# Kernel tuning notes

Hardware: AMD Instinct MI355X
Metric: run time of the kernel (lower is better)

## Reference

```python
import jax, jax.numpy as jnp
import numpy as np

B, L, K = 4, 2048, 30
NS, NV = 1024, 256   # node hidden (scalar, vector)
ES, EV = 32, 1       # edge hidden (scalar, vector)
CLAMP = 32           # clamp_rel_pos
PE = 16              # num positional embeddings

def _nan_to_num(t):
    return jnp.where(jnp.isfinite(t), t, jnp.zeros((), t.dtype))

def _norm(t, axis=-1, keepdims=False, eps=1e-8):
    return jnp.sqrt(jnp.sum(t * t, axis=axis, keepdims=keepdims) + eps)

def _normalize(t, axis=-1):
    return _nan_to_num(t / _norm(t, axis=axis, keepdims=True))

def _norm_no_nan(t, axis=-1, keepdims=False, eps=1e-8, sqrt=True):
    out = jnp.maximum(jnp.sum(t * t, axis=axis, keepdims=keepdims), eps)
    return jnp.sqrt(out) if sqrt else out

def _rbf(values, v_min, v_max, n_bins=16):
    centers = jnp.linspace(v_min, v_max, n_bins)
    std = (v_max - v_min) / n_bins
    z = (values[..., None] - centers) / std
    return jnp.exp(-z * z)

def _dihedrals(X, eps=1e-7):
    b = X.shape[0]
    Xf = X[:, :, :3].reshape(b, -1, 3)           # [B, 3L, 3]
    U = _normalize(Xf[:, 1:] - Xf[:, :-1])
    u2, u1, u0 = U[:, :-2], U[:, 1:-1], U[:, 2:]
    n2 = _normalize(jnp.cross(u2, u1))
    n1 = _normalize(jnp.cross(u1, u0))
    cosD = jnp.clip(jnp.sum(n2 * n1, -1), -1 + eps, 1 - eps)
    D = jnp.sign(jnp.sum(u2 * n1, -1)) * jnp.arccos(cosD)
    D = jnp.pad(D, ((0, 0), (1, 2))).reshape(b, -1, 3)
    return jnp.concatenate([jnp.cos(D), jnp.sin(D)], -1)   # [B,L,6]

def _orientations(Xca):
    f = jnp.pad(_normalize(Xca[:, 1:] - Xca[:, :-1]), ((0, 0), (0, 1), (0, 0)))
    bk = jnp.pad(_normalize(Xca[:, :-1] - Xca[:, 1:]), ((0, 0), (1, 0), (0, 0)))
    return jnp.concatenate([f[:, :, None], bk[:, :, None]], -2)  # [B,L,2,3]

def _sidechains(X):
    n, origin, c = X[:, :, 0], X[:, :, 1], X[:, :, 2]
    c, n = _normalize(c - origin), _normalize(n - origin)
    bisector = _normalize(c + n)
    perp = _normalize(jnp.cross(c, n))
    return -bisector * float(np.sqrt(1.0 / 3.0)) - perp * float(np.sqrt(2.0 / 3.0))

def _dist(Xca, coord_mask, res_idx, padding_mask, k, order=3):
    n = Xca.shape[1]
    cmf = coord_mask.astype(jnp.float32)
    cm2 = cmf[:, None, :] * cmf[:, :, None]
    rmf = (~padding_mask).astype(jnp.float32)
    rm2 = rmf[:, None, :] * rmf[:, :, None]
    dX = Xca[:, None, :, :] - Xca[:, :, None, :]
    D = cm2 * _norm(dX, axis=-1)
    cov = (jnp.abs(res_idx[:, :, None] - res_idx[:, None, :]) <= order).astype(jnp.float32)
    D_cov = D * (1.0 - cov)
    seqpos = jnp.arange(n)
    Dseq = jnp.abs(seqpos[:, None] - seqpos[None, :]).astype(jnp.float32)
    D_adjust = _nan_to_num(D_cov) + (1.0 - cm2) * (1e8 + Dseq * 1e6) + (1.0 - rm2) * 1e10
    _, E_idx = jax.lax.top_k(-D_adjust, k)                # k smallest
    D_neighbors = jnp.take_along_axis(D, E_idx, axis=-1)  # regather raw D (as in source)
    return D_neighbors, E_idx, D_neighbors < 5e7, D_neighbors < 5e9

def _edge_features(coords, coord_mask, res_idx, padding_mask):
    Xca = coords[:, :, 1]
    E_dist, E_idx, E_cm, E_rm = _dist(Xca, coord_mask, res_idx, padding_mask, K)
    b, n, k = E_idx.shape
    src = jnp.broadcast_to(jnp.arange(n, dtype=E_idx.dtype)[None, :, None], (b, n, k))
    edge_index = jnp.stack([src, E_idx], 0).reshape(2, b, n * k)
    E_dist = E_dist.reshape(b, n * k)
    E_cm = E_cm.reshape(b, n * k)
    E_rm = E_rm.reshape(b, n * k)
    E_cmf = E_cm[..., None].astype(jnp.float32)
    edge_start = jnp.take_along_axis(res_idx, edge_index[0], axis=-1)
    edge_end = jnp.take_along_axis(res_idx, edge_index[1], axis=-1)
    d = jnp.clip(edge_start - edge_end, -CLAMP, CLAMP).astype(jnp.float32)
    freq = jnp.exp(jnp.arange(0, PE, 2, dtype=jnp.float32) * (-np.log(10000.0) / PE))
    ang = d[..., None] * freq
    pos = jnp.concatenate([jnp.cos(ang), jnp.sin(ang)], -1)
    D_rbf = _rbf(E_dist, 0.0, 20.0)
    X_src = jnp.broadcast_to(Xca[:, :, None, :], (b, n, k, 3)).reshape(b, n * k, 3)
    X_dest = jnp.take_along_axis(Xca, edge_index[1][..., None], axis=1)
    cm_src = jnp.broadcast_to(coord_mask[:, :, None], (b, n, k)).reshape(b, n * k)
    cm_dest = jnp.take_along_axis(coord_mask, edge_index[1], axis=1)
    E_vec = X_src - X_dest
    E_mean = jnp.sum(E_vec * E_cmf, 1, keepdims=True) / jnp.sum(E_cmf, 1, keepdims=True)
    E_vec = E_vec * E_cmf + E_mean * (1.0 - E_cmf)
    edge_s = _nan_to_num(jnp.concatenate([D_rbf, pos], -1))
    edge_v = _nan_to_num(_normalize(E_vec)[:, :, None, :])
    edge_s = jnp.concatenate([edge_s,
                              (~cm_src).astype(jnp.float32)[..., None],
                              (~cm_dest).astype(jnp.float32)[..., None]], -1)  # [B,Lk,34]
    invalid = (~E_rm) | (~E_cm)   # remove_edges_without_coords=True
    edge_index = jnp.where(invalid[None], -1, edge_index)
    return edge_s, edge_v, jnp.transpose(edge_index, (1, 0, 2)), invalid

def _gvp(s, v, wh, ws_w, ws_b, wv):
    # v: [..., vi, 3]; activations=(None, None), vector_gate=False
    vh = jnp.einsum('...id,ih->...hd', v, wh)       # [..., h, 3]
    vn = _norm_no_nan(vh, axis=-1)                  # [..., h]
    s_out = jnp.concatenate([s, vn], -1) @ ws_w + ws_b
    v_out = jnp.einsum('...hd,hv->...vd', vh, wv)
    return s_out, v_out

def _gvp_layernorm(s, v, gamma, beta, eps=1e-4):
    mu = jnp.mean(s, -1, keepdims=True)
    var = jnp.mean((s - mu) ** 2, -1, keepdims=True)
    s_out = (s - mu) / jnp.sqrt(var + eps) * gamma + beta
    vn2 = _norm_no_nan(v, axis=-1, keepdims=True, sqrt=False)
    v_out = v / jnp.sqrt(jnp.mean(vn2, axis=-2, keepdims=True))
    return s_out, v_out

def _forward(coords, coord_mask, res_idx, padding_mask, confidence,
             node_wh, node_ws_w, node_ws_b, node_wv, node_ln_g, node_ln_b,
             edge_wh, edge_ws_w, edge_ws_b, edge_wv, edge_ln_g, edge_ln_b,
             conf_w, conf_b):
    node_s = jnp.concatenate([_dihedrals(coords),
                              coord_mask.astype(jnp.float32)[..., None]], -1)  # [B,L,7]
    node_v = jnp.concatenate([_orientations(coords[:, :, 1]),
                              _sidechains(coords)[:, :, None]], -2)            # [B,L,3,3]
    edge_s, edge_v, edge_index, invalid = _edge_features(coords, coord_mask, res_idx, padding_mask)
    # torch.no_grad() over featurization
    node_s, node_v, edge_s, edge_v = map(jax.lax.stop_gradient,
                                         (node_s, node_v, edge_s, edge_v))
    ns, nv = _gvp_layernorm(*_gvp(node_s, node_v, node_wh, node_ws_w, node_ws_b, node_wv),
                            node_ln_g, node_ln_b)
    es, ev = _gvp_layernorm(*_gvp(edge_s, edge_v, edge_wh, edge_ws_w, edge_ws_b, edge_wv),
                            edge_ln_g, edge_ln_b)
    ns = ns + _rbf(confidence, 0.0, 1.0) @ conf_w + conf_b
    b = ns.shape[0]
    ns = ns.reshape(b * L, NS)
    nv = nv.reshape(b * L, NV, 3)
    es = es.reshape(b * L * K, ES)
    ev = ev.reshape(b * L * K, EV, 3)
    # flatten_graph (padded: invalid edges kept with index -1, embeddings zeroed)
    valid = (~invalid).reshape(-1)
    ei = edge_index + (jnp.arange(b, dtype=edge_index.dtype) * L)[:, None, None]
    ei = jnp.transpose(ei, (1, 0, 2)).reshape(2, -1)
    ei = jnp.where(valid[None, :], ei, -1)
    es = jnp.where(valid[:, None], es, 0.0)
    ev = jnp.where(valid[:, None, None], ev, 0.0)
    return ns, nv, es, ev, ei

def setup_inputs():
    key = jax.random.key(0)
    ks = jax.random.split(key, 12)
    def lin(k, fan_in, shape):
        return jax.random.normal(k, shape, jnp.float32) / np.sqrt(fan_in)
    return {
        'coords': jax.random.normal(ks[0], (B, L, 3, 3), jnp.float32),
        'coord_mask': jax.random.randint(ks[1], (B, L), 0, 2) > 0,
        'res_idx': jnp.arange(B * L, dtype=jnp.int32).reshape(B, L),
        'padding_mask': jnp.zeros((B, L), dtype=bool),
        'confidence': jax.random.uniform(ks[2], (B, L), jnp.float32),
        'node_wh': lin(ks[3], 3, (3, NV)),
        'node_ws_w': lin(ks[4], NV + 7, (NV + 7, NS)),
        'node_ws_b': jnp.zeros((NS,), jnp.float32),
        'node_wv': lin(ks[5], NV, (NV, NV)),
        'node_ln_g': jnp.ones((NS,), jnp.float32),
        'node_ln_b': jnp.zeros((NS,), jnp.float32),
        'edge_wh': lin(ks[6], 1, (1, 1)),
        'edge_ws_w': lin(ks[7], 35, (35, ES)),
        'edge_ws_b': jnp.zeros((ES,), jnp.float32),
        'edge_wv': lin(ks[8], 1, (1, 1)),
        'edge_ln_g': jnp.ones((ES,), jnp.float32),
        'edge_ln_b': jnp.zeros((ES,), jnp.float32),
        'conf_w': lin(ks[9], 16, (16, NS)),
        'conf_b': jnp.zeros((NS,), jnp.float32),
    }

def reference(coords, coord_mask, res_idx, padding_mask, confidence,
              node_wh, node_ws_w, node_ws_b, node_wv, node_ln_g, node_ln_b,
              edge_wh, edge_ws_w, edge_ws_b, edge_wv, edge_ln_g, edge_ln_b,
              conf_w, conf_b):
    return _forward(coords, coord_mask, res_idx, padding_mask, confidence,
                    node_wh, node_ws_w, node_ws_b, node_wv, node_ln_g, node_ln_b,
                    edge_wh, edge_ws_w, edge_ws_b, edge_wv, edge_ln_g, edge_ln_b,
                    conf_w, conf_b)
```

## Files before the change

kernel.cpp:

```cpp
#include <hip/hip_runtime.h>
#include <math.h>

constexpr int Bc = 4, Lc = 2048, Kc = 30;
constexpr int Nn = Bc * Lc;
constexpr int NSc = 1024, NVc = 256;
constexpr int NEc = Nn * Kc;
constexpr int SK = 263;

constexpr size_t OUT_NS = 0;
constexpr size_t OUT_NV = (size_t)Nn * NSc;
constexpr size_t OUT_ES = OUT_NV + (size_t)Nn * NVc * 3;
constexpr size_t OUT_EV = OUT_ES + (size_t)NEc * 32;
constexpr size_t OUT_EI = OUT_EV + (size_t)NEc * 3;

constexpr size_t WS_SIN = 0;
constexpr size_t WS_NDV = WS_SIN + (size_t)Nn * SK;
constexpr size_t WS_EIX = WS_NDV + (size_t)Nn * 9;
constexpr size_t WS_EDS = WS_EIX + (size_t)NEc;
constexpr size_t WS_CMF = WS_EDS + (size_t)NEc;

__device__ __forceinline__ void norml3(float& x, float& y, float& z) {
  float ss = x*x + y*y + z*z;
  float inv = 1.0f / sqrtf(ss + 1e-8f);
  x *= inv; y *= inv; z *= inv;
}

__global__ __launch_bounds__(256) void kinit(const unsigned char* __restrict__ cm,
                                             const float* __restrict__ coords,
                                             const int* __restrict__ resid,
                                             const unsigned char* __restrict__ pmask,
                                             const float* __restrict__ wh,
                                             const float* __restrict__ wv,
                                             float* __restrict__ ws,
                                             float4* __restrict__ pack,
                                             float4* __restrict__ whwv4,
                                             float4* __restrict__ wht4) {
  __shared__ float r0[256], r1[256], r2[256];
  __shared__ int flag;
  int tid = threadIdx.x;
  if (blockIdx.x < 32) {
    if (tid == 0) flag = 0;
    __syncthreads();
    int any = 0;
    for (int p = tid; p < 1024; p += 256)
      if (p & 3) any |= cm[p];
    if (any) atomicOr(&flag, 1);
    __syncthreads();
    bool bytefmt = (flag != 0);
    int n = blockIdx.x * 256 + tid;
    unsigned char v = bytefmt ? cm[n] : cm[4*n];
    ws[WS_CMF + n] = v ? 1.f : 0.f;
    int rm = (pmask[n] == 0) ? 1 : 0;
    int w = (resid[n] << 2) | ((v ? 1 : 0) << 1) | rm;
    float4 p;
    p.x = coords[(size_t)n*9 + 3];
    p.y = coords[(size_t)n*9 + 4];
    p.z = coords[(size_t)n*9 + 5];
    p.w = __int_as_float(w);
    pack[n] = p;
  } else {
    int lane = tid & 63, wid = tid >> 6;
    int vcol = (int)(blockIdx.x - 32) * 64 + lane;
    float a0 = 0.f, a1 = 0.f, a2 = 0.f;
    #pragma unroll 4
    for (int hh = 0; hh < 64; ++hh) {
      int h = wid * 64 + hh;
      float wvv = wv[(size_t)h * 256 + vcol];
      a0 = fmaf(wh[h],       wvv, a0);
      a1 = fmaf(wh[256 + h], wvv, a1);
      a2 = fmaf(wh[512 + h], wvv, a2);
    }
    r0[tid] = a0; r1[tid] = a1; r2[tid] = a2;
    __syncthreads();
    if (wid == 0) {
      a0 = r0[lane] + r0[lane+64] + r0[lane+128] + r0[lane+192];
      a1 = r1[lane] + r1[lane+64] + r1[lane+128] + r1[lane+192];
      a2 = r2[lane] + r2[lane+64] + r2[lane+128] + r2[lane+192];
      whwv4[vcol] = float4{a0, a1, a2, 0.f};
    } else if (wid == 1) {
      wht4[vcol] = float4{wh[vcol], wh[256 + vcol], wh[512 + vcol], 0.f};
    }
  }
}

__global__ __launch_bounds__(64) void knode_geom(const float* __restrict__ coords,
                                                 float* __restrict__ ws) {
  int n = blockIdx.x * 64 + threadIdx.x;
  if (n >= Nn) return;
  int b = n / Lc, l = n % Lc;
  const float* Xb = coords + (size_t)b * Lc * 9;
  float ax[7][3];
  #pragma unroll
  for (int m = 0; m < 7; ++m) {
    int t = 3*l + m - 2;
    if (t >= 0 && t < 3*Lc) { ax[m][0]=Xb[t*3+0]; ax[m][1]=Xb[t*3+1]; ax[m][2]=Xb[t*3+2]; }
    else { ax[m][0]=0.f; ax[m][1]=0.f; ax[m][2]=0.f; }
  }
  float U[5][3];
  #pragma unroll
  for (int mi = 0; mi < 5; ++mi) {
    int t = 3*l - 1 + mi;
    if (t >= 0 && t <= 3*Lc - 2) {
      float x = ax[mi+2][0]-ax[mi+1][0], y = ax[mi+2][1]-ax[mi+1][1], z = ax[mi+2][2]-ax[mi+1][2];
      norml3(x,y,z);
      U[mi][0]=x; U[mi][1]=y; U[mi][2]=z;
    } else { U[mi][0]=0.f; U[mi][1]=0.f; U[mi][2]=0.f; }
  }
  float cph[3], sph[3];
  #pragma unroll
  for (int a = 0; a < 3; ++a) {
    int t = 3*l + a - 1;
    if (t < 0 || t > 3*Lc - 4) { cph[a] = 1.f; sph[a] = 0.f; continue; }
    const float *u2 = U[a], *u1 = U[a+1], *u0 = U[a+2];
    float n2x = u2[1]*u1[2]-u2[2]*u1[1], n2y = u2[2]*u1[0]-u2[0]*u1[2], n2z = u2[0]*u1[1]-u2[1]*u1[0];
    norml3(n2x,n2y,n2z);
    float n1x = u1[1]*u0[2]-u1[2]*u0[1], n1y = u1[2]*u0[0]-u1[0]*u0[2], n1z = u1[0]*u0[1]-u1[1]*u0[0];
    norml3(n1x,n1y,n1z);
    float cd = n2x*n1x + n2y*n1y + n2z*n1z;
    cd = fminf(fmaxf(cd, -1.f + 1e-7f), 1.f - 1e-7f);
    float dt = u2[0]*n1x + u2[1]*n1y + u2[2]*n1z;
    float sg = (dt > 0.f) ? 1.f : ((dt < 0.f) ? -1.f : 0.f);
    float D = sg * acosf(cd);
    cph[a] = cosf(D); sph[a] = sinf(D);
  }
  float fx=0.f,fy=0.f,fz=0.f, kx=0.f,ky=0.f,kz=0.f;
  if (l < Lc-1) { fx=ax[6][0]-ax[3][0]; fy=ax[6][1]-ax[3][1]; fz=ax[6][2]-ax[3][2]; norml3(fx,fy,fz); }
  if (l > 0)    { kx=ax[0][0]-ax[3][0]; ky=ax[0][1]-ax[3][1]; kz=ax[0][2]-ax[3][2]; norml3(kx,ky,kz); }
  float cx=ax[4][0]-ax[3][0], cy=ax[4][1]-ax[3][1], cz=ax[4][2]-ax[3][2]; norml3(cx,cy,cz);
  float nx=ax[2][0]-ax[3][0], ny=ax[2][1]-ax[3][1], nz=ax[2][2]-ax[3][2]; norml3(nx,ny,nz);
  float bix=cx+nx, biy=cy+ny, biz=cz+nz; norml3(bix,biy,biz);
  float px=cy*nz-cz*ny, py=cz*nx-cx*nz, pz=cx*ny-cy*nx; norml3(px,py,pz);
  const float c1 = 0.57735026f, c2 = 0.81649658f;
  float sx = -bix*c1 - px*c2, sy = -biy*c1 - py*c2, sz = -biz*c1 - pz*c2;

  float cmf = ws[WS_CMF + n];
  float* sr = ws + WS_SIN + (size_t)n * SK;
  sr[0]=cph[0]; sr[1]=cph[1]; sr[2]=cph[2]; sr[3]=sph[0]; sr[4]=sph[1]; sr[5]=sph[2]; sr[6]=cmf;
  float* vr = ws + WS_NDV + (size_t)n * 9;
  vr[0]=fx; vr[1]=fy; vr[2]=fz; vr[3]=kx; vr[4]=ky; vr[5]=kz; vr[6]=sx; vr[7]=sy; vr[8]=sz;
}

__global__ __launch_bounds__(256) void kvnode(const float4* __restrict__ wht4,
                                              const float4* __restrict__ whwv4,
                                              float* __restrict__ ws,
                                              float* __restrict__ out) {
  int tid = threadIdx.x, lane = tid & 63, wid = tid >> 6;
  int n = blockIdx.x * 4 + wid;
  const float* v = ws + WS_NDV + (size_t)n * 9;
  float v00=v[0],v01=v[1],v02=v[2];
  float v10=v[3],v11=v[4],v12=v[5];
  float v20=v[6],v21=v[7],v22=v[8];
  float p = 0.f;
  float vo[4][3];
  #pragma unroll
  for (int m = 0; m < 4; ++m) {
    int hv = lane + 64*m;
    float4 wt = wht4[hv];
    float vh0 = v00*wt.x + v10*wt.y + v20*wt.z;
    float vh1 = v01*wt.x + v11*wt.y + v21*wt.z;
    float vh2 = v02*wt.x + v12*wt.y + v22*wt.z;
    ws[WS_SIN + (size_t)n*SK + 7 + hv] = sqrtf(fmaxf(vh0*vh0 + vh1*vh1 + vh2*vh2, 1e-8f));
    int ho = lane*4 + m;
    float4 wc = whwv4[ho];
    float o0 = v00*wc.x + v10*wc.y + v20*wc.z;
    float o1 = v01*wc.x + v11*wc.y + v21*wc.z;
    float o2 = v02*wc.x + v12*wc.y + v22*wc.z;
    vo[m][0]=o0; vo[m][1]=o1; vo[m][2]=o2;
    p += fmaxf(o0*o0 + o1*o1 + o2*o2, 1e-8f);
  }
  #pragma unroll
  for (int off = 1; off < 64; off <<= 1) p += __shfl_xor(p, off);
  float isd = 1.f / sqrtf(p * (1.f/256.f));
  size_t o = OUT_NV + (size_t)n*768 + (size_t)lane*12;
  float4 f0 = {vo[0][0]*isd, vo[0][1]*isd, vo[0][2]*isd, vo[1][0]*isd};
  float4 f1 = {vo[1][1]*isd, vo[1][2]*isd, vo[2][0]*isd, vo[2][1]*isd};
  float4 f2 = {vo[2][2]*isd, vo[3][0]*isd, vo[3][1]*isd, vo[3][2]*isd};
  *(float4*)&out[o+0] = f0;
  *(float4*)&out[o+4] = f1;
  *(float4*)&out[o+8] = f2;
}

__global__ __launch_bounds__(256) void ktopk(const float4* __restrict__ pack,
                                             float* __restrict__ ws) {
  __shared__ unsigned long long cbuf[4][256];
  int tid = threadIdx.x, lane = tid & 63, wid = tid >> 6;
  int row = blockIdx.x * 4 + wid;
  int b = row >> 11;
  int i = row & (Lc - 1);
  const float4* P = pack + (size_t)b * Lc;
  int* eix = (int*)(ws + WS_EIX);
  unsigned long long lmask_lt = (1ULL << lane) - 1ULL;

  float4 pi = P[i];
  int wi = __float_as_int(pi.w);
  float cmi = ((wi >> 1) & 1) ? 1.f : 0.f;
  float rmi = (wi & 1) ? 1.f : 0.f;
  int ri = wi >> 2;

  unsigned a[32];
  unsigned lmin = 0xFFFFFFFFu;
  #pragma unroll
  for (int half = 0; half < 2; ++half) {
    float4 pjs[16];
    #pragma unroll
    for (int q = 0; q < 16; ++q)
      pjs[q] = P[lane + 64*(half*16 + q)];
    #pragma unroll
    for (int q = 0; q < 16; ++q) {
      int m = half*16 + q;
      int j = lane + 64*m;
      float4 pj = pjs[q];
      int wj = __float_as_int(pj.w);
      float cmj = ((wj >> 1) & 1) ? 1.f : 0.f;
      float rmj = (wj & 1) ? 1.f : 0.f;
      float dx = __fsub_rn(pi.x, pj.x);
      float dy = __fsub_rn(pi.y, pj.y);
      float dz = __fsub_rn(pi.z, pj.z);
      float ss = __fadd_rn(__fadd_rn(__fmul_rn(dx,dx), __fmul_rn(dy,dy)), __fmul_rn(dz,dz));
      float dist = __fsqrt_rn(__fadd_rn(ss, 1e-8f));
      float cm2 = __fmul_rn(cmi, cmj);
      float D = __fmul_rn(cm2, dist);
      int ad = ri - (wj >> 2); ad = ad < 0 ? -ad : ad;
      float covm = (ad <= 3) ? 0.f : 1.f;
      float dseq = (float)(i >= j ? i - j : j - i);
      float t1 = __fmul_rn(__fsub_rn(1.f, cm2), __fadd_rn(1e8f, __fmul_rn(dseq, 1e6f)));
      float rm2 = __fmul_rn(rmi, rmj);
      float t2 = __fmul_rn(__fsub_rn(1.f, rm2), 1e10f);
      float adj = __fadd_rn(__fadd_rn(__fmul_rn(D, covm), t1), t2);
      unsigned u = __float_as_uint(adj);
      a[m] = u;
      lmin = u < lmin ? u : lmin;
    }
  }

  unsigned lo = 0u, hi = 0x51000000u;
  while (lo < hi) {
    unsigned mid = lo + ((hi - lo) >> 1);
    unsigned long long bal = __ballot(lmin <= mid);
    if (__popcll(bal) >= Kc) hi = mid; else lo = mid + 1u;
  }
  unsigned Tv = lo;

  unsigned base = 0;
  #pragma unroll
  for (int m = 0; m < 32; ++m) {
    bool pred = (a[m] <= Tv);
    unsigned long long bal = __ballot(pred);
    if (pred) {
      unsigned pos = base + (unsigned)__popcll(bal & lmask_lt);
      if (pos < 256u)
        cbuf[wid][pos] = ((unsigned long long)a[m] << 32) | (unsigned)(lane + 64*m);
    }
    base += (unsigned)__popcll(bal);
  }
  unsigned M = base < 256u ? base : 256u;
  __builtin_amdgcn_wave_barrier();

  for (unsigned idx = (unsigned)lane; idx < M; idx += 64u) {
    unsigned long long k0 = cbuf[wid][idx];
    int rank = 0;
    for (unsigned t = 0; t < M; ++t) rank += (cbuf[wid][t] < k0) ? 1 : 0;
    if (rank < Kc) {
      int j = (int)(k0 & 2047ULL);
      float4 pj = P[j];
      int wj = __float_as_int(pj.w);
      float cmj = ((wj >> 1) & 1) ? 1.f : 0.f;
      float dx = __fsub_rn(pi.x, pj.x);
      float dy = __fsub_rn(pi.y, pj.y);
      float dz = __fsub_rn(pi.z, pj.z);
      float ss2 = __fadd_rn(__fadd_rn(__fmul_rn(dx,dx), __fmul_rn(dy,dy)), __fmul_rn(dz,dz));
      float dist = __fsqrt_rn(__fadd_rn(ss2, 1e-8f));
      float D = __fmul_rn(__fmul_rn(cmi, cmj), dist);
      eix[(size_t)row*Kc + rank] = j;
      ws[WS_EDS + (size_t)row*Kc + rank] = D;
    }
  }
}

__global__ __launch_bounds__(256) void kgemm_s(const float* __restrict__ ws,
                                               const float* __restrict__ wsw,
                                               const float* __restrict__ wsb,
                                               float* __restrict__ out) {
  __shared__ __align__(16) float As[32][132];
  __shared__ __align__(16) float Bs[32][64];
  int tid = threadIdx.x;
  int lb = (int)(blockIdx.x & 7) * 128 + (int)(blockIdx.x >> 3);
  int by = lb >> 4, bx = lb & 15;
  int row0 = by * 128, cn0 = bx * 64;
  int tx = tid & 15, ty = tid >> 4;
  int aka = tid & 15, arw = tid >> 4;
  int bkk = tid >> 4, bc4 = tid & 15;
  const float* Abase = ws + WS_SIN;

  float ar[16];
  float4 br[2];
  #pragma unroll
  for (int h = 0; h < 2; ++h) {
    int ka = h*16 + aka;
    #pragma unroll
    for (int i = 0; i < 8; ++i)
      ar[h*8+i] = Abase[(size_t)(row0 + arw + 16*i)*SK + ka];
    br[h] = *(const float4*)&wsw[(size_t)(h*16 + bkk)*NSc + cn0 + bc4*4];
  }
  float acc[8][4] = {};
  for (int k0 = 0; k0 < SK; k0 += 32) {
    #pragma unroll
    for (int h = 0; h < 2; ++h) {
      #pragma unroll
      for (int i = 0; i < 8; ++i)
        As[h*16 + aka][arw + 16*i] = ar[h*8+i];
      *(float4*)&Bs[h*16 + bkk][bc4*4] = br[h];
    }
    __syncthreads();
    int kn = k0 + 32;
    if (kn < SK) {
      #pragma unroll
      for (int h = 0; h < 2; ++h) {
        int ka = kn + h*16 + aka;
        bool ok = (ka < SK);
        #pragma unroll
        for (int i = 0; i < 8; ++i)
          ar[h*8+i] = ok ? Abase[(size_t)(row0 + arw + 16*i)*SK + ka] : 0.f;
        int kb = kn + h*16 + bkk;
        br[h] = (kb < SK) ? *(const float4*)&wsw[(size_t)kb*NSc + cn0 + bc4*4]
                          : float4{0.f,0.f,0.f,0.f};
      }
    }
    #pragma unroll 4
    for (int kk = 0; kk < 32; ++kk) {
      float4 a0 = *(const float4*)&As[kk][ty*8 + 0];
      float4 a1 = *(const float4*)&As[kk][ty*8 + 4];
      float4 b4 = *(const float4*)&Bs[kk][tx*4];
      float av[8] = {a0.x,a0.y,a0.z,a0.w, a1.x,a1.y,a1.z,a1.w};
      float bv[4] = {b4.x,b4.y,b4.z,b4.w};
      #pragma unroll
      for (int r = 0; r < 8; ++r)
        #pragma unroll
        for (int c = 0; c < 4; ++c)
          acc[r][c] = fmaf(av[r], bv[c], acc[r][c]);
    }
    __syncthreads();
  }
  float4 bb = *(const float4*)&wsb[cn0 + tx*4];
  #pragma unroll
  for (int r = 0; r < 8; ++r) {
    size_t o = OUT_NS + (size_t)(row0 + ty*8 + r)*NSc + cn0 + tx*4;
    float4 ov = {acc[r][0]+bb.x, acc[r][1]+bb.y, acc[r][2]+bb.z, acc[r][3]+bb.w};
    *(float4*)&out[o] = ov;
  }
}

__global__ __launch_bounds__(256) void kedge(const float* __restrict__ coords,
    const int* __restrict__ resid,
    const float* __restrict__ ewh, const float* __restrict__ eww,
    const float* __restrict__ ewb, const float* __restrict__ ewv,
    const float* __restrict__ elg, const float* __restrict__ elb,
    const float* __restrict__ ws, float* __restrict__ out) {
  __shared__ float w[35*32];
  __shared__ float wb[32], g[32], bb[32];
  __shared__ float es[256*33];
  int tid = threadIdx.x;
  for (int t = tid; t < 35*32; t += 256) w[t] = eww[t];
  if (tid < 32) { wb[tid] = ewb[tid]; g[tid] = elg[tid]; bb[tid] = elb[tid]; }
  __syncthreads();
  int e = blockIdx.x * 256 + tid;
  int b = e / (Lc*Kc);
  int rem = e - b*(Lc*Kc);
  int i = rem / Kc;
  int row = b*Lc + i;
  const int* eix = (const int*)(ws + WS_EIX);
  int j = eix[e];
  float Dn = ws[WS_EDS + e];
  bool jok = ((unsigned)j < (unsigned)Lc);
  bool valid = jok && (Dn < 5e7f) && (Dn < 5e9f);
  int sj = jok ? j : 0;

  int dcl = resid[row] - resid[b*Lc + sj];
  dcl = dcl < -32 ? -32 : (dcl > 32 ? 32 : dcl);
  float dpos = (float)dcl;
  float s[35];
  #pragma unroll
  for (int m = 0; m < 16; ++m) {
    float c = (20.f/15.f) * (float)m;
    float z = (Dn - c) * 0.8f;
    s[m] = expf(-z*z);
  }
  #pragma unroll
  for (int m = 0; m < 8; ++m) {
    float fr = expf((float)(2*m) * (-0.57564627324851148f));
    float ang = dpos * fr;
    s[16+m] = cosf(ang);
    s[24+m] = sinf(ang);
  }
  float csf = ws[WS_CMF + row];
  float cdf = ws[WS_CMF + b*Lc + sj];
  s[32] = 1.f - csf; s[33] = 1.f - cdf;
  const float* Xb = coords + (size_t)b*Lc*9;
  float vx = Xb[i*9+3] - Xb[sj*9+3];
  float vy = Xb[i*9+4] - Xb[sj*9+4];
  float vz = Xb[i*9+5] - Xb[sj*9+5];
  float ss2 = vx*vx + vy*vy + vz*vz;
  float inv = 1.f / sqrtf(ss2 + 1e-8f);
  float e0 = vx*inv, e1 = vy*inv, e2 = vz*inv;
  if (!isfinite(e0)) e0 = 0.f;
  if (!isfinite(e1)) e1 = 0.f;
  if (!isfinite(e2)) e2 = 0.f;
  float wh00 = ewh[0], wv00 = ewv[0];
  float vh0 = e0*wh00, vh1 = e1*wh00, vh2 = e2*wh00;
  s[34] = sqrtf(fmaxf(vh0*vh0 + vh1*vh1 + vh2*vh2, 1e-8f));
  float o[32]; float sm = 0.f;
  #pragma unroll
  for (int c = 0; c < 32; ++c) {
    float a = wb[c];
    #pragma unroll
    for (int q = 0; q < 35; ++q) a = fmaf(s[q], w[q*32 + c], a);
    o[c] = a; sm += a;
  }
  float mu = sm * (1.f/32.f);
  float sq = 0.f;
  #pragma unroll
  for (int c = 0; c < 32; ++c) { float dd = o[c]-mu; sq += dd*dd; }
  float isd = 1.f / sqrtf(sq*(1.f/32.f) + 1e-4f);
  float vo0 = vh0*wv00, vo1 = vh1*wv00, vo2 = vh2*wv00;
  float vn2 = fmaxf(vo0*vo0 + vo1*vo1 + vo2*vo2, 1e-8f);
  float ivn = 1.f / sqrtf(vn2);

  #pragma unroll
  for (int c = 0; c < 32; ++c)
    es[tid*33 + c] = valid ? ((o[c]-mu)*isd*g[c] + bb[c]) : 0.f;
  out[OUT_EI + e]       = valid ? (float)row : -1.f;
  out[OUT_EI + NEc + e] = valid ? (float)(b*Lc + j) : -1.f;
  __syncthreads();
  {
    size_t base32 = OUT_ES + (size_t)blockIdx.x * 256 * 32;
    #pragma unroll
    for (int k = 0; k < 8; ++k) {
      int flat = (k*256 + tid) * 4;
      int el = flat >> 5, c0 = flat & 31;
      float4 vq = {es[el*33+c0], es[el*33+c0+1], es[el*33+c0+2], es[el*33+c0+3]};
      *(float4*)&out[base32 + flat] = vq;
    }
  }
  __syncthreads();
  es[tid*3 + 0] = valid ? vo0*ivn : 0.f;
  es[tid*3 + 1] = valid ? vo1*ivn : 0.f;
  es[tid*3 + 2] = valid ? vo2*ivn : 0.f;
  __syncthreads();
  if (tid < 192) {
    size_t base3 = OUT_EV + (size_t)blockIdx.x * 768;
    float4 vq = {es[tid*4], es[tid*4+1], es[tid*4+2], es[tid*4+3]};
    *(float4*)&out[base3 + tid*4] = vq;
  }
}

__global__ __launch_bounds__(256) void kln_node(const float* __restrict__ conf,
    const float* __restrict__ cw, const float* __restrict__ cb,
    const float* __restrict__ lg, const float* __restrict__ lb,
    float* __restrict__ out) {
  int n = blockIdx.x, tid = threadIdx.x;
  size_t base = OUT_NS + (size_t)n*NSc;
  float x0 = out[base + tid];
  float x1 = out[base + tid + 256];
  float x2 = out[base + tid + 512];
  float x3 = out[base + tid + 768];
  float sm = x0+x1+x2+x3;
  float sq = x0*x0+x1*x1+x2*x2+x3*x3;
  int lane = tid & 63, wid = tid >> 6;
  #pragma unroll
  for (int off = 32; off > 0; off >>= 1) { sm += __shfl_down(sm, off); sq += __shfl_down(sq, off); }
  __shared__ float rs[4], rq[4];
  if (lane == 0) { rs[wid] = sm; rq[wid] = sq; }
  __syncthreads();
  sm = rs[0]+rs[1]+rs[2]+rs[3];
  sq = rq[0]+rq[1]+rq[2]+rq[3];
  float mu = sm * (1.f/1024.f);
  float var = fmaxf(sq * (1.f/1024.f) - mu*mu, 0.f);
  float isd = 1.f / sqrtf(var + 1e-4f);
  float cf = conf[n];
  float rb[16];
  #pragma unroll
  for (int m = 0; m < 16; ++m) {
    float z = (cf - (float)m*(1.f/15.f)) * 16.f;
    rb[m] = expf(-z*z);
  }
  float xs_[4] = {x0, x1, x2, x3};
  #pragma unroll
  for (int q = 0; q < 4; ++q) {
    int c = tid + q*256;
    float t = cb[c];
    #pragma unroll
    for (int m = 0; m < 16; ++m) t = fmaf(rb[m], cw[m*1024 + c], t);
    out[base + c] = (xs_[q]-mu)*isd*lg[c] + lb[c] + t;
  }
}

extern "C" void kernel_launch(void* const* d_in, const int* in_sizes, int n_in,
                              void* d_out, int out_size, void* d_ws, size_t ws_size,
                              hipStream_t stream) {
  const float* coords         = (const float*)d_in[0];
  const unsigned char* cmask  = (const unsigned char*)d_in[1];
  const int* resid            = (const int*)d_in[2];
  const unsigned char* pmask  = (const unsigned char*)d_in[3];
  const float* conf           = (const float*)d_in[4];
  const float* nwh            = (const float*)d_in[5];
  const float* nww            = (const float*)d_in[6];
  const float* nwb            = (const float*)d_in[7];
  const float* nwv            = (const float*)d_in[8];
  const float* nlg            = (const float*)d_in[9];
  const float* nlb            = (const float*)d_in[10];
  const float* ewh            = (const float*)d_in[11];
  const float* eww            = (const float*)d_in[12];
  const float* ewb            = (const float*)d_in[13];
  const float* ewv            = (const float*)d_in[14];
  const float* elg            = (const float*)d_in[15];
  const float* elb            = (const float*)d_in[16];
  const float* cw             = (const float*)d_in[17];
  const float* cb             = (const float*)d_in[18];
  float* out = (float*)d_out;
  float* ws  = (float*)d_ws;
  float4* whwv4 = (float4*)(out + OUT_ES);
  float4* wht4  = whwv4 + 256;
  float4* pack  = (float4*)(out + OUT_EV);

  kinit<<<36, 256, 0, stream>>>(cmask, coords, resid, pmask, nwh, nwv, ws, pack, whwv4, wht4);
  knode_geom<<<Nn/64, 64, 0, stream>>>(coords, ws);
  kvnode<<<Nn/4, 256, 0, stream>>>(wht4, whwv4, ws, out);
  ktopk<<<Nn/4, 256, 0, stream>>>(pack, ws);
  kgemm_s<<<(Nn/128)*(NSc/64), 256, 0, stream>>>(ws, nww, nwb, out);
  kedge<<<NEc/256, 256, 0, stream>>>(coords, resid, ewh, eww, ewb, ewv, elg, elb, ws, out);
  kln_node<<<Nn, 256, 0, stream>>>(conf, cw, cb, nlg, nlb, out);
}
```

Measured before the change: 285.7 us.

## Move node scalar GEMM to bf16x3 split MFMA with padded pre-converted operands

Replaces the fp32 FMA tiled GEMM for the node scalar projection with a matrix-core version. Each fp32 operand is split into high and low bf16 halves and three MFMA products are summed to keep near-fp32 accuracy. Two new prep kernels convert A and a transposed B into the padded (K=288) bf16 layouts, stored in scratch space inside the output's edge region before kedge overwrites it. This adds two extra launches and extra memory traffic, and dropping the lo*lo term slightly reduces accuracy.

```diff
diff --git a/kernel.cpp b/kernel.cpp
--- a/kernel.cpp
+++ b/kernel.cpp
@@ -6,6 +6,7 @@
 constexpr int NSc = 1024, NVc = 256;
 constexpr int NEc = Nn * Kc;
 constexpr int SK = 263;
+constexpr int KP = 288;
 
 constexpr size_t OUT_NS = 0;
 constexpr size_t OUT_NV = (size_t)Nn * NSc;
@@ -19,10 +20,22 @@
 constexpr size_t WS_EDS = WS_EIX + (size_t)NEc;
 constexpr size_t WS_CMF = WS_EDS + (size_t)NEc;
 
+using short8 = __attribute__((ext_vector_type(8))) short;
+using f32x4  = __attribute__((ext_vector_type(4))) float;
+
 __device__ __forceinline__ void norml3(float& x, float& y, float& z) {
   float ss = x*x + y*y + z*z;
   float inv = 1.0f / sqrtf(ss + 1e-8f);
   x *= inv; y *= inv; z *= inv;
+}
+
+__device__ __forceinline__ void bf16split(float x, unsigned short& h, unsigned short& l) {
+  unsigned u = __float_as_uint(x);
+  unsigned hb = (u + 0x7FFFu + ((u >> 16) & 1u)) & 0xFFFF0000u;
+  float lf = x - __uint_as_float(hb);
+  unsigned ul = __float_as_uint(lf);
+  h = (unsigned short)(hb >> 16);
+  l = (unsigned short)((ul + 0x7FFFu + ((ul >> 16) & 1u)) >> 16);
 }
 
 __global__ __launch_bounds__(256) void kinit(const unsigned char* __restrict__ cm,
@@ -277,77 +290,111 @@
   }
 }
 
-__global__ __launch_bounds__(256) void kgemm_s(const float* __restrict__ ws,
-                                               const float* __restrict__ wsw,
+__global__ __launch_bounds__(64) void kprepA(const float* __restrict__ ws,
+                                             unsigned short* __restrict__ Ahi,
+                                             unsigned short* __restrict__ Alo) {
+  int n = blockIdx.x, t = threadIdx.x;
+  const float* src = ws + WS_SIN + (size_t)n * SK;
+  size_t dst = (size_t)n * KP;
+  #pragma unroll
+  for (int p = 0; p < 5; ++p) {
+    int k = t + 64*p;
+    if (k >= KP) break;
+    float x = (k < SK) ? src[k] : 0.f;
+    unsigned short h, l;
+    bf16split(x, h, l);
+    Ahi[dst + k] = h;
+    Alo[dst + k] = l;
+  }
+}
+
+__global__ __launch_bounds__(256) void kprepB(const float* __restrict__ wsw,
+                                              unsigned short* __restrict__ Bhi,
+                                              unsigned short* __restrict__ Blo) {
+  __shared__ float tile[32][33];
+  int bidx = blockIdx.x;
+  int kt = bidx % 9, ct = bidx / 9;
+  int k0 = kt*32, c0 = ct*32;
+  int t = threadIdx.x;
+  int r = t >> 5, c = t & 31;
+  #pragma unroll
+  for (int p = 0; p < 4; ++p) {
+    int k = k0 + r + 8*p;
+    tile[r + 8*p][c] = (k < SK) ? wsw[(size_t)k*NSc + c0 + c] : 0.f;
+  }
+  __syncthreads();
+  int cc = t >> 3, kq = (t & 7) * 4;
+  ushort4 h4, l4;
+  float x0 = tile[kq+0][cc], x1 = tile[kq+1][cc], x2 = tile[kq+2][cc], x3 = tile[kq+3][cc];
+  bf16split(x0, h4.x, l4.x);
+  bf16split(x1, h4.y, l4.y);
+  bf16split(x2, h4.z, l4.z);
+  bf16split(x3, h4.w, l4.w);
+  size_t o = (size_t)(c0 + cc) * KP + k0 + kq;
+  *(ushort4*)&Bhi[o] = h4;
+  *(ushort4*)&Blo[o] = l4;
+}
+
+__global__ __launch_bounds__(256) void kgemm_s(const unsigned short* __restrict__ Ahi,
+                                               const unsigned short* __restrict__ Alo,
+                                               const unsigned short* __restrict__ Bhi,
+                                               const unsigned short* __restrict__ Blo,
                                                const float* __restrict__ wsb,
                                                float* __restrict__ out) {
-  __shared__ __align__(16) float As[32][132];
-  __shared__ __align__(16) float Bs[32][64];
-  int tid = threadIdx.x;
+  __shared__ __align__(16) unsigned short Ah[64][40], Al[64][40];
+  __shared__ __align__(16) unsigned short Bh[128][40], Bl[128][40];
+  int tid = threadIdx.x, lane = tid & 63, w = tid >> 6;
   int lb = (int)(blockIdx.x & 7) * 128 + (int)(blockIdx.x >> 3);
-  int by = lb >> 4, bx = lb & 15;
-  int row0 = by * 128, cn0 = bx * 64;
-  int tx = tid & 15, ty = tid >> 4;
-  int aka = tid & 15, arw = tid >> 4;
-  int bkk = tid >> 4, bc4 = tid & 15;
-  const float* Abase = ws + WS_SIN;
-
-  float ar[16];
-  float4 br[2];
-  #pragma unroll
-  for (int h = 0; h < 2; ++h) {
-    int ka = h*16 + aka;
-    #pragma unroll
-    for (int i = 0; i < 8; ++i)
-      ar[h*8+i] = Abase[(size_t)(row0 + arw + 16*i)*SK + ka];
-    br[h] = *(const float4*)&wsw[(size_t)(h*16 + bkk)*NSc + cn0 + bc4*4];
-  }
-  float acc[8][4] = {};
-  for (int k0 = 0; k0 < SK; k0 += 32) {
-    #pragma unroll
-    for (int h = 0; h < 2; ++h) {
+  int by = lb >> 3, bx = lb & 7;
+  int row0 = by * 64, cn0 = bx * 128;
+  int wr = w & 1, wc = w >> 1;
+  int sar = tid >> 2, sak = (tid & 3) * 8;
+  int sbc = tid >> 1, sbk = (tid & 1) * 16;
+  int fr = lane & 15, kq = (lane >> 4) * 8;
+  f32x4 acc[2][4] = {};
+
+  for (int ks = 0; ks < 9; ++ks) {
+    int k0 = ks * 32;
+    *(uint4*)&Ah[sar][sak] = *(const uint4*)&Ahi[(size_t)(row0+sar)*KP + k0 + sak];
+    *(uint4*)&Al[sar][sak] = *(const uint4*)&Alo[(size_t)(row0+sar)*KP + k0 + sak];
+    *(uint4*)&Bh[sbc][sbk]     = *(const uint4*)&Bhi[(size_t)(cn0+sbc)*KP + k0 + sbk];
+    *(uint4*)&Bh[sbc][sbk + 8] = *(const uint4*)&Bhi[(size_t)(cn0+sbc)*KP + k0 + sbk + 8];
+    *(uint4*)&Bl[sbc][sbk]     = *(const uint4*)&Blo[(size_t)(cn0+sbc)*KP + k0 + sbk];
+    *(uint4*)&Bl[sbc][sbk + 8] = *(const uint4*)&Blo[(size_t)(cn0+sbc)*KP + k0 + sbk + 8];
+    __syncthreads();
+    short8 ah[2], alr[2], bh[4], blr[4];
+    #pragma unroll
+    for (int rg = 0; rg < 2; ++rg) {
+      ah[rg]  = *(const short8*)&Ah[wr*32 + rg*16 + fr][kq];
+      alr[rg] = *(const short8*)&Al[wr*32 + rg*16 + fr][kq];
+    }
+    #pragma unroll
+    for (int cg = 0; cg < 4; ++cg) {
+      bh[cg]  = *(const short8*)&Bh[wc*64 + cg*16 + fr][kq];
+      blr[cg] = *(const short8*)&Bl[wc*64 + cg*16 + fr][kq];
+    }
+    #pragma unroll
+    for (int rg = 0; rg < 2; ++rg)
       #pragma unroll
-      for (int i = 0; i < 8; ++i)
-        As[h*16 + aka][arw + 16*i] = ar[h*8+i];
-      *(float4*)&Bs[h*16 + bkk][bc4*4] = br[h];
-    }
+      for (int cg = 0; cg < 4; ++cg) {
+        acc[rg][cg] = __builtin_amdgcn_mfma_f32_16x16x32_bf16(ah[rg],  bh[cg],  acc[rg][cg], 0, 0, 0);
+        acc[rg][cg] = __builtin_amdgcn_mfma_f32_16x16x32_bf16(ah[rg],  blr[cg], acc[rg][cg], 0, 0, 0);
+        acc[rg][cg] = __builtin_amdgcn_mfma_f32_16x16x32_bf16(alr[rg], bh[cg],  acc[rg][cg], 0, 0, 0);
+      }
     __syncthreads();
-    int kn = k0 + 32;
-    if (kn < SK) {
+  }
+  #pragma unroll
+  for (int rg = 0; rg < 2; ++rg)
+    #pragma unroll
+    for (int cg = 0; cg < 4; ++cg) {
+      int col = cn0 + wc*64 + cg*16 + fr;
+      float bb = wsb[col];
       #pragma unroll
-      for (int h = 0; h < 2; ++h) {
-        int ka = kn + h*16 + aka;
-        bool ok = (ka < SK);
-        #pragma unroll
-        for (int i = 0; i < 8; ++i)
-          ar[h*8+i] = ok ? Abase[(size_t)(row0 + arw + 16*i)*SK + ka] : 0.f;
-        int kb = kn + h*16 + bkk;
-        br[h] = (kb < SK) ? *(const float4*)&wsw[(size_t)kb*NSc + cn0 + bc4*4]
-                          : float4{0.f,0.f,0.f,0.f};
+      for (int q = 0; q < 4; ++q) {
+        int row = row0 + wr*32 + rg*16 + (lane >> 4)*4 + q;
+        out[OUT_NS + (size_t)row*NSc + col] = acc[rg][cg][q] + bb;
       }
     }
-    #pragma unroll 4
-    for (int kk = 0; kk < 32; ++kk) {
-      float4 a0 = *(const float4*)&As[kk][ty*8 + 0];
-      float4 a1 = *(const float4*)&As[kk][ty*8 + 4];
-      float4 b4 = *(const float4*)&Bs[kk][tx*4];
-      float av[8] = {a0.x,a0.y,a0.z,a0.w, a1.x,a1.y,a1.z,a1.w};
-      float bv[4] = {b4.x,b4.y,b4.z,b4.w};
-      #pragma unroll
-      for (int r = 0; r < 8; ++r)
-        #pragma unroll
-        for (int c = 0; c < 4; ++c)
-          acc[r][c] = fmaf(av[r], bv[c], acc[r][c]);
-    }
-    __syncthreads();
-  }
-  float4 bb = *(const float4*)&wsb[cn0 + tx*4];
-  #pragma unroll
-  for (int r = 0; r < 8; ++r) {
-    size_t o = OUT_NS + (size_t)(row0 + ty*8 + r)*NSc + cn0 + tx*4;
-    float4 ov = {acc[r][0]+bb.x, acc[r][1]+bb.y, acc[r][2]+bb.z, acc[r][3]+bb.w};
-    *(float4*)&out[o] = ov;
-  }
 }
 
 __global__ __launch_bounds__(256) void kedge(const float* __restrict__ coords,
@@ -518,15 +565,22 @@
   const float* cb             = (const float*)d_in[18];
   float* out = (float*)d_out;
   float* ws  = (float*)d_ws;
-  float4* whwv4 = (float4*)(out + OUT_ES);
+  float* esbase = out + OUT_ES;
+  float4* whwv4 = (float4*)esbase;
   float4* wht4  = whwv4 + 256;
+  unsigned short* Ahi = (unsigned short*)(esbase + 2048);
+  unsigned short* Alo = Ahi + (size_t)Nn * KP;
+  unsigned short* BhiT = Alo + (size_t)Nn * KP;
+  unsigned short* BloT = BhiT + (size_t)NSc * KP;
   float4* pack  = (float4*)(out + OUT_EV);
 
   kinit<<<36, 256, 0, stream>>>(cmask, coords, resid, pmask, nwh, nwv, ws, pack, whwv4, wht4);
   knode_geom<<<Nn/64, 64, 0, stream>>>(coords, ws);
   kvnode<<<Nn/4, 256, 0, stream>>>(wht4, whwv4, ws, out);
   ktopk<<<Nn/4, 256, 0, stream>>>(pack, ws);
-  kgemm_s<<<(Nn/128)*(NSc/64), 256, 0, stream>>>(ws, nww, nwb, out);
+  kprepA<<<Nn, 64, 0, stream>>>(ws, Ahi, Alo);
+  kprepB<<<288, 256, 0, stream>>>(nww, BhiT, BloT);
+  kgemm_s<<<(Nn/64)*(NSc/128), 256, 0, stream>>>(Ahi, Alo, BhiT, BloT, nwb, out);
   kedge<<<NEc/256, 256, 0, stream>>>(coords, resid, ewh, eww, ewb, ewv, elg, elb, ws, out);
   kln_node<<<Nn, 256, 0, stream>>>(conf, cw, cb, nlg, nlb, out);
 }
```

Result: faster. 257.0 us (-10.0%).
